# Kernel tuning notes

Hardware: AMD Instinct MI355X
Metric: run time of the kernel (lower is better)

## Reference

```python
import jax, jax.numpy as jnp
import numpy as np

EMBED_DIM = 512
NUM_HEADS = 8
HEAD_DIM = EMBED_DIM // NUM_HEADS
LN_EPS = 1e-5


def setup_inputs() -> dict:
    key = jax.random.key(0)
    ks = jax.random.split(key, 14)
    B, Lq, Lkv, E = 4, 1024, 4096, EMBED_DIM
    s = 0.02
    return {
        "query": jax.random.normal(ks[0], (B, Lq, E), dtype=jnp.float32),
        "key_value": jax.random.normal(ks[1], (B, Lkv, E), dtype=jnp.float32),
        "w_q": jax.random.normal(ks[2], (E, E), dtype=jnp.float32) * s,
        "w_k": jax.random.normal(ks[3], (E, E), dtype=jnp.float32) * s,
        "w_v": jax.random.normal(ks[4], (E, E), dtype=jnp.float32) * s,
        "b_q": jnp.zeros((E,), dtype=jnp.float32),
        "b_k": jnp.zeros((E,), dtype=jnp.float32),
        "b_v": jnp.zeros((E,), dtype=jnp.float32),
        "w_o": jax.random.normal(ks[5], (E, E), dtype=jnp.float32) * s,
        "b_o": jnp.zeros((E,), dtype=jnp.float32),
        "ln_gamma": jnp.ones((E,), dtype=jnp.float32),
        "ln_beta": jnp.zeros((E,), dtype=jnp.float32),
    }


def reference(query, key_value, w_q, w_k, w_v, b_q, b_k, b_v, w_o, b_o, ln_gamma, ln_beta):
    # query: [B, Lq, E]; key_value: [B, Lkv, E]
    B, Lq, E = query.shape
    Lkv = key_value.shape[1]
    H, D = NUM_HEADS, HEAD_DIM

    q = (query @ w_q.T + b_q).reshape(B, Lq, H, D)
    k = (key_value @ w_k.T + b_k).reshape(B, Lkv, H, D)
    v = (key_value @ w_v.T + b_v).reshape(B, Lkv, H, D)

    scale = 1.0 / jnp.sqrt(jnp.asarray(D, dtype=query.dtype))
    scores = jnp.einsum("bqhd,bkhd->bhqk", q, k) * scale  # [B,H,Lq,Lkv]
    attn = jax.nn.softmax(scores, axis=-1)
    # attn dropout off (eval mode)

    ctx = jnp.einsum("bhqk,bkhd->bqhd", attn, v).reshape(B, Lq, E)
    attn_output = ctx @ w_o.T + b_o
    # post-attn dropout off (eval mode)

    x = query + attn_output
    mu = jnp.mean(x, axis=-1, keepdims=True)
    var = jnp.mean(jnp.square(x - mu), axis=-1, keepdims=True)
    out = (x - mu) / jnp.sqrt(var + LN_EPS) * ln_gamma + ln_beta

    # need_weights=True: PyTorch averages attention weights over heads
    attn_weights = jnp.mean(attn, axis=1)  # [B, Lq, Lkv]
    return out, attn_weights
```

## Files before the change

kernel.cpp:

```cpp
#include <hip/hip_runtime.h>
#include <hip/hip_bf16.h>

namespace {

constexpr int E_DIM = 512;
constexpr int NH = 8;
constexpr int HD = 64;
constexpr int LQ = 1024;
constexpr int LKV = 4096;
constexpr int NB = 4;
constexpr int SPLIT = 4;
constexpr int SLICE = LKV / SPLIT;
constexpr int SSPLIT = 8;
constexpr size_t CPL = (size_t)NB * LQ * E_DIM;

typedef __attribute__((ext_vector_type(8))) short bf16x8;
typedef __attribute__((ext_vector_type(8))) unsigned short u16x8;
typedef __attribute__((ext_vector_type(4))) float f32x4;

typedef const unsigned int __attribute__((address_space(1)))* gptr1;
typedef unsigned int __attribute__((address_space(3)))* lptr3;

__device__ __forceinline__ void gl16(const unsigned short* g, unsigned short* l) {
  __builtin_amdgcn_global_load_lds((gptr1)g, (lptr3)l, 16, 0, 0);
}

__device__ __forceinline__ f32x4 mfma16(bf16x8 a, bf16x8 b, f32x4 c) {
  return __builtin_amdgcn_mfma_f32_16x16x32_bf16(a, b, c, 0, 0, 0);
}

__device__ __forceinline__ unsigned short f2b(float f) {
  unsigned int u = __float_as_uint(f);
  u += 0x7FFFu + ((u >> 16) & 1u);
  return (unsigned short)(u >> 16);
}

__device__ __forceinline__ float b2f(short s) {
  return __uint_as_float(((unsigned int)(unsigned short)s) << 16);
}

__device__ __forceinline__ unsigned int cvt_pk_bf16(float a, float b) {
  unsigned int r;
  asm("v_cvt_pk_bf16_f32 %0, %1, %2" : "=v"(r) : "v"(a), "v"(b));
  return r;
}

__global__ __launch_bounds__(256) void cvt_bf16(const float* __restrict__ s,
                                                unsigned short* __restrict__ d) {
  const int i = blockIdx.x * 256 + threadIdx.x;
  const float4 a = ((const float4*)s)[i * 2];
  const float4 b = ((const float4*)s)[i * 2 + 1];
  uint4 o;
  o.x = cvt_pk_bf16(a.x, a.y);
  o.y = cvt_pk_bf16(a.z, a.w);
  o.z = cvt_pk_bf16(b.x, b.y);
  o.w = cvt_pk_bf16(b.z, b.w);
  ((uint4*)d)[i] = o;
}

__global__ __launch_bounds__(256) void cvt_w4(const float* __restrict__ w0,
                                              const float* __restrict__ w1,
                                              const float* __restrict__ w2,
                                              const float* __restrict__ w3,
                                              unsigned short* __restrict__ d) {
  const float* s = blockIdx.y == 0 ? w0 : blockIdx.y == 1 ? w1
                   : blockIdx.y == 2 ? w2 : w3;
  unsigned short* dst = d + (size_t)blockIdx.y * (E_DIM * E_DIM);
  const int i = blockIdx.x * 256 + threadIdx.x;
  const float4 a = ((const float4*)s)[i * 2];
  const float4 b = ((const float4*)s)[i * 2 + 1];
  uint4 o;
  o.x = cvt_pk_bf16(a.x, a.y);
  o.y = cvt_pk_bf16(a.z, a.w);
  o.z = cvt_pk_bf16(b.x, b.y);
  o.w = cvt_pk_bf16(b.z, b.w);
  ((uint4*)dst)[i] = o;
}

template <int EPI>
__global__ __launch_bounds__(256) void gemm_bf16(
    const unsigned short* __restrict__ A, const unsigned short* __restrict__ B,
    const float* __restrict__ bias, void* __restrict__ outp, int L,
    float oscale) {
  __shared__ __align__(16) unsigned short As[128][32];
  __shared__ __align__(16) unsigned short Bs[128][32];
  const int tid = threadIdx.x;
  const int wv = tid >> 6, lane = tid & 63, lg = lane >> 4, lr = lane & 15;
  const int gx = gridDim.x, gy = gridDim.y;
  const int p = blockIdx.x + gx * blockIdx.y;
  const int xcd = p & 7, ii = p >> 3;
  const int by = xcd * (gy >> 3) + ii / gx;
  const int bx = ii - (ii / gx) * gx;
  const int i0 = by * 128, j0 = bx * 128;
  const int wm = wv >> 1, wn = wv & 1;
  const int srow = tid >> 2, scol = (tid & 3) * 8;
  f32x4 acc[4][4] = {};
  const unsigned short* ap = A + (size_t)(i0 + srow) * E_DIM + scol;
  const unsigned short* bp = B + (size_t)(j0 + srow) * E_DIM + scol;
  unsigned short* lA = &As[srow][scol];
  unsigned short* lB = &Bs[srow][scol];
  for (int k0 = 0; k0 < E_DIM; k0 += 32) {
    __syncthreads();
    gl16(ap + k0, lA);
    gl16(ap + k0 + (size_t)64 * E_DIM, lA + 64 * 32);
    gl16(bp + k0, lB);
    gl16(bp + k0 + (size_t)64 * E_DIM, lB + 64 * 32);
    __syncthreads();
    bf16x8 af[4], bg[4];
    for (int m = 0; m < 4; ++m)
      af[m] = *(const bf16x8*)&As[wm * 64 + m * 16 + lr][lg * 8];
    for (int n = 0; n < 4; ++n)
      bg[n] = *(const bf16x8*)&Bs[wn * 64 + n * 16 + lr][lg * 8];
    for (int m = 0; m < 4; ++m)
      for (int n = 0; n < 4; ++n)
        acc[m][n] = mfma16(af[m], bg[n], acc[m][n]);
  }
  for (int m = 0; m < 4; ++m)
    for (int n = 0; n < 4; ++n) {
      const int j = j0 + wn * 64 + n * 16 + lr;
      const float bj = bias[j];
      for (int r = 0; r < 4; ++r) {
        const int i = i0 + wm * 64 + m * 16 + lg * 4 + r;
        const float v = (acc[m][n][r] + bj) * oscale;
        if (EPI == 2) {
          ((float*)outp)[(size_t)i * E_DIM + j] = v;
        } else {
          const int bb = i / L, li = i - bb * L;
          const int hh = j >> 6, dd = j & 63;
          if (EPI == 0)
            ((unsigned short*)outp)[((size_t)(bb * NH + hh) * L + li) * HD + dd] = f2b(v);
          else
            ((unsigned short*)outp)[((size_t)(bb * NH + hh) * HD + dd) * L + li] = f2b(v);
        }
      }
    }
}

__global__ __launch_bounds__(512, 2) void attn_sums(
    const unsigned short* __restrict__ Qb, const unsigned short* __restrict__ Kb,
    float* __restrict__ l_part) {
  const int tid = threadIdx.x;
  const int h = tid >> 6, lane = tid & 63, lg = lane >> 4, lr = lane & 15;
  const int p = blockIdx.x + 16 * blockIdx.y + 64 * blockIdx.z;
  const int xcd = p & 7, ii = p >> 3;
  const int combo = xcd * 4 + (ii >> 4);
  const int q0 = (ii & 15) * 64;
  const int b = combo >> 3, sp = combo & 7;
  const size_t bh = (size_t)b * NH + h;
  const unsigned short* Qp = Qb + (bh * LQ + q0) * HD;
  const unsigned short* Kp = Kb + (bh * LKV + sp * (LKV / SSPLIT)) * HD;
  bf16x8 qB[4][2];
  for (int qs = 0; qs < 4; ++qs)
    for (int kk = 0; kk < 2; ++kk)
      qB[qs][kk] = *(const bf16x8*)(Qp + (qs * 16 + lr) * HD + kk * 32 + lg * 8);
  float qsum[4] = {};
  for (int t = 0; t < (LKV / SSPLIT) / 64; ++t) {
    const unsigned short* base = Kp + (size_t)t * 64 * HD;
    for (int k2h = 0; k2h < 2; ++k2h) {
      bf16x8 kA[2][2];
      for (int k2 = 0; k2 < 2; ++k2)
        for (int kk = 0; kk < 2; ++kk)
          kA[k2][kk] = *(const bf16x8*)(base + ((k2h * 2 + k2) * 16 + lr) * HD +
                                        kk * 32 + lg * 8);
      f32x4 sacc[2][4] = {};
      for (int k2 = 0; k2 < 2; ++k2)
        for (int qs = 0; qs < 4; ++qs)
          sacc[k2][qs] = mfma16(kA[k2][1], qB[qs][1],
                                mfma16(kA[k2][0], qB[qs][0], sacc[k2][qs]));
      for (int k2 = 0; k2 < 2; ++k2)
        for (int qs = 0; qs < 4; ++qs)
          for (int r = 0; r < 4; ++r)
            qsum[qs] += __builtin_amdgcn_exp2f(sacc[k2][qs][r]);
    }
  }
  for (int qs = 0; qs < 4; ++qs) {
    float v = qsum[qs];
    v += __shfl_xor(v, 16);
    v += __shfl_xor(v, 32);
    if (lg == 0)
      l_part[(size_t)sp * (NB * NH * LQ) + bh * LQ + q0 + qs * 16 + lr] = v;
  }
}

__global__ __launch_bounds__(512) void attn_main(
    const unsigned short* __restrict__ Qb, const unsigned short* __restrict__ Kb,
    const unsigned short* __restrict__ Vt, const float* __restrict__ l_part,
    float* __restrict__ attn_w, unsigned short* __restrict__ ctxp) {
  __shared__ __align__(16) unsigned short P[2][NH][64][72];
  const int tid = threadIdx.x;
  const int h = tid >> 6, lane = tid & 63, lg = lane >> 4, lr = lane & 15;
  const int p = blockIdx.x + 16 * blockIdx.y + 64 * blockIdx.z;
  const int xcd = p & 7, ii = p >> 3;
  const int combo = xcd * 2 + (ii >> 4);
  const int q0 = (ii & 15) * 64;
  const int b = combo >> 2, sp = combo & 3;
  const size_t bh = (size_t)b * NH + h;
  const unsigned short* Qp = Qb + (bh * LQ + q0) * HD;
  const unsigned short* Kp = Kb + bh * LKV * HD;
  const unsigned short* Vp = Vt + bh * HD * LKV;

  bf16x8 qB[4][2];
  for (int qs = 0; qs < 4; ++qs)
    for (int kk = 0; kk < 2; ++kk)
      qB[qs][kk] = *(const bf16x8*)(Qp + (qs * 16 + lr) * HD + kk * 32 + lg * 8);
  float nlg[4];
  for (int qs = 0; qs < 4; ++qs) {
    float ls = 0.f;
    for (int s = 0; s < SSPLIT; ++s)
      ls += l_part[(size_t)s * (NB * NH * LQ) + bh * LQ + q0 + qs * 16 + lr];
    nlg[qs] = -__builtin_amdgcn_logf(ls);
  }

  f32x4 cacc[4][4] = {};
  for (int t = 0; t < SLICE / 64; ++t) {
    const int kv0 = sp * SLICE + t * 64;
    unsigned short (*Pb)[64][72] = P[t & 1];
    bf16x8 vf[4][2];
    for (int ds = 0; ds < 4; ++ds)
      for (int kk = 0; kk < 2; ++kk)
        vf[ds][kk] = *(const bf16x8*)(Vp + (size_t)(ds * 16 + lr) * LKV + kv0 +
                                      kk * 32 + lg * 8);
    for (int kh = 0; kh < 2; ++kh) {
      bf16x8 kA[2][2];
      for (int k2 = 0; k2 < 2; ++k2)
        for (int kk = 0; kk < 2; ++kk)
          kA[k2][kk] = *(const bf16x8*)(Kp + (size_t)(kv0 + (kh * 2 + k2) * 16 + lr) * HD +
                                        kk * 32 + lg * 8);
      f32x4 sacc[2][4] = {};
      for (int k2 = 0; k2 < 2; ++k2)
        for (int qs = 0; qs < 4; ++qs)
          sacc[k2][qs] = mfma16(kA[k2][1], qB[qs][1],
                                mfma16(kA[k2][0], qB[qs][0], sacc[k2][qs]));
      for (int k2 = 0; k2 < 2; ++k2)
        for (int qs = 0; qs < 4; ++qs) {
          const int q = qs * 16 + lr;
          const float p0 = __builtin_amdgcn_exp2f(sacc[k2][qs][0] + nlg[qs]);
          const float p1 = __builtin_amdgcn_exp2f(sacc[k2][qs][1] + nlg[qs]);
          const float p2 = __builtin_amdgcn_exp2f(sacc[k2][qs][2] + nlg[qs]);
          const float p3 = __builtin_amdgcn_exp2f(sacc[k2][qs][3] + nlg[qs]);
          uint2 w;
          w.x = cvt_pk_bf16(p0, p1);
          w.y = cvt_pk_bf16(p2, p3);
          *(uint2*)&Pb[h][q][(kh * 2 + k2) * 16 + lg * 4] = w;
        }
    }
    for (int kk = 0; kk < 2; ++kk) {
      bf16x8 pa[4];
      for (int qs = 0; qs < 4; ++qs)
        pa[qs] = *(const bf16x8*)&Pb[h][qs * 16 + lr][kk * 32 + lg * 8];
      for (int qs = 0; qs < 4; ++qs)
        for (int ds = 0; ds < 4; ++ds)
          cacc[qs][ds] = mfma16(pa[qs], vf[ds][kk], cacc[qs][ds]);
    }
    __syncthreads();
    {
      const int qa = tid >> 3, La = tid & 7;
      float s[8] = {};
      for (int hh = 0; hh < NH; ++hh) {
        const bf16x8 v = *(const bf16x8*)&Pb[hh][qa][La * 8];
        for (int j = 0; j < 8; ++j) s[j] += b2f(v[j]);
      }
      float* op = attn_w + (size_t)(b * LQ + q0 + qa) * LKV + kv0 + La * 8;
      float4 o0 = {s[0] * 0.125f, s[1] * 0.125f, s[2] * 0.125f, s[3] * 0.125f};
      float4 o1 = {s[4] * 0.125f, s[5] * 0.125f, s[6] * 0.125f, s[7] * 0.125f};
      *(float4*)op = o0;
      *(float4*)(op + 4) = o1;
    }
  }
  unsigned short* cp = ctxp + (size_t)sp * CPL;
  for (int qs = 0; qs < 4; ++qs)
    for (int ds = 0; ds < 4; ++ds)
      for (int r = 0; r < 4; ++r)
        cp[(size_t)(b * LQ + q0 + qs * 16 + lg * 4 + r) * E_DIM + h * HD +
           ds * 16 + lr] = f2b(cacc[qs][ds][r]);
}

__global__ __launch_bounds__(256) void combine_ctx(
    const unsigned short* __restrict__ ctxp, unsigned short* __restrict__ ctxb) {
  const size_t i = (size_t)blockIdx.x * 256 + threadIdx.x;
  float s[8] = {};
  for (int pl = 0; pl < SPLIT; ++pl) {
    const bf16x8 v = ((const bf16x8*)(ctxp + pl * CPL))[i];
    for (int j = 0; j < 8; ++j) s[j] += b2f(v[j]);
  }
  uint4 o;
  o.x = cvt_pk_bf16(s[0], s[1]);
  o.y = cvt_pk_bf16(s[2], s[3]);
  o.z = cvt_pk_bf16(s[4], s[5]);
  o.w = cvt_pk_bf16(s[6], s[7]);
  ((uint4*)ctxb)[i] = o;
}

__global__ __launch_bounds__(256) void ln_kernel(
    const float* __restrict__ q, const float* __restrict__ ao,
    const float* __restrict__ gamma, const float* __restrict__ beta,
    float* __restrict__ out) {
  const int row = blockIdx.x;
  const int tid = threadIdx.x;
  const size_t base = (size_t)row * E_DIM;
  const float x0 = q[base + tid] + ao[base + tid];
  const float x1 = q[base + 256 + tid] + ao[base + 256 + tid];
  float s = x0 + x1, ss = x0 * x0 + x1 * x1;
  for (int off = 32; off >= 1; off >>= 1) {
    s += __shfl_down(s, off);
    ss += __shfl_down(ss, off);
  }
  __shared__ float ps[4], pss[4];
  if ((tid & 63) == 0) {
    ps[tid >> 6] = s;
    pss[tid >> 6] = ss;
  }
  __syncthreads();
  s = ps[0] + ps[1] + ps[2] + ps[3];
  ss = pss[0] + pss[1] + pss[2] + pss[3];
  const float mu = s * (1.f / E_DIM);
  float var = ss * (1.f / E_DIM) - mu * mu;
  var = fmaxf(var, 0.f);
  const float rstd = rsqrtf(var + 1e-5f);
  out[base + tid] = (x0 - mu) * rstd * gamma[tid] + beta[tid];
  out[base + 256 + tid] = (x1 - mu) * rstd * gamma[256 + tid] + beta[256 + tid];
}

}

extern "C" void kernel_launch(void* const* d_in, const int* in_sizes, int n_in,
                              void* d_out, int out_size, void* d_ws, size_t ws_size,
                              hipStream_t stream) {
  const float* query = (const float*)d_in[0];
  const float* key_value = (const float*)d_in[1];
  const float* w_q = (const float*)d_in[2];
  const float* w_k = (const float*)d_in[3];
  const float* w_v = (const float*)d_in[4];
  const float* b_q = (const float*)d_in[5];
  const float* b_k = (const float*)d_in[6];
  const float* b_v = (const float*)d_in[7];
  const float* w_o = (const float*)d_in[8];
  const float* b_o = (const float*)d_in[9];
  const float* ln_g = (const float*)d_in[10];
  const float* ln_b = (const float*)d_in[11];

  unsigned short* Qb = (unsigned short*)d_ws;
  unsigned short* Kb = Qb + 2097152;
  unsigned short* Vt = Kb + 8388608;
  float* l_part = (float*)(Vt + 8388608);
  unsigned short* Wb = (unsigned short*)(l_part + 262144);
  float* ao = (float*)(Wb + 1048576);
  unsigned short* KVb = (unsigned short*)(ao + 2097152);
  unsigned short* ctxp = KVb;
  unsigned short* Qxb = KVb + 8388608;
  unsigned short* ctxb = Qxb;

  float* out = (float*)d_out;
  float* attn_w = out + (size_t)NB * LQ * E_DIM;

  const float qscale = 0.125f * 1.44269504088896340736f;

  cvt_bf16<<<dim3(4096), dim3(256), 0, stream>>>(key_value, KVb);
  cvt_bf16<<<dim3(1024), dim3(256), 0, stream>>>(query, Qxb);
  cvt_w4<<<dim3(128, 4), dim3(256), 0, stream>>>(w_q, w_k, w_v, w_o, Wb);

  gemm_bf16<0><<<dim3(4, 32), dim3(256), 0, stream>>>(Qxb, Wb, b_q, Qb, LQ, qscale);
  gemm_bf16<0><<<dim3(4, 128), dim3(256), 0, stream>>>(KVb, Wb + 262144, b_k, Kb,
                                                       LKV, 1.0f);
  gemm_bf16<1><<<dim3(4, 128), dim3(256), 0, stream>>>(KVb, Wb + 524288, b_v, Vt,
                                                       LKV, 1.0f);

  attn_sums<<<dim3(16, NB, SSPLIT), dim3(512), 0, stream>>>(Qb, Kb, l_part);
  attn_main<<<dim3(16, NB, SPLIT), dim3(512), 0, stream>>>(Qb, Kb, Vt, l_part,
                                                           attn_w, ctxp);
  combine_ctx<<<dim3(1024), dim3(256), 0, stream>>>(ctxp, ctxb);
  gemm_bf16<2><<<dim3(4, 32), dim3(256), 0, stream>>>(ctxb, Wb + 786432, b_o, ao,
                                                      LQ, 1.0f);
  ln_kernel<<<dim3(NB * LQ), dim3(256), 0, stream>>>(query, ao, ln_g, ln_b, out);
}
```

Before: 257.0 us.

## Double KV split in attention, single-buffer P for occupancy, merge conversion kernels

Doubles the KV split of attn_main from 4 to 8 slices, which doubles the grid. The per-block LDS buffer for P is single-buffered, with an extra barrier, so that two 512-thread blocks can fit per CU, and the kernel requests that with launch bounds. The three fp32-to-bf16 conversion kernels are merged into one launch, and the bf16 unpacking in the head-average and combine steps uses plain bit masks. In exchange, combine_ctx reads twice as many partial contexts, the larger partial buffer spills over the staged query copy (so ctxb is moved onto Qb), and each tile adds a sync.

```diff
diff --git a/kernel.cpp b/kernel.cpp
--- a/kernel.cpp
+++ b/kernel.cpp
@@ -9,7 +9,7 @@
 constexpr int LQ = 1024;
 constexpr int LKV = 4096;
 constexpr int NB = 4;
-constexpr int SPLIT = 4;
+constexpr int SPLIT = 8;
 constexpr int SLICE = LKV / SPLIT;
 constexpr int SSPLIT = 8;
 constexpr size_t CPL = (size_t)NB * LQ * E_DIM;
@@ -35,46 +35,43 @@
   return (unsigned short)(u >> 16);
 }
 
-__device__ __forceinline__ float b2f(short s) {
-  return __uint_as_float(((unsigned int)(unsigned short)s) << 16);
-}
-
 __device__ __forceinline__ unsigned int cvt_pk_bf16(float a, float b) {
   unsigned int r;
   asm("v_cvt_pk_bf16_f32 %0, %1, %2" : "=v"(r) : "v"(a), "v"(b));
   return r;
 }
 
-__global__ __launch_bounds__(256) void cvt_bf16(const float* __restrict__ s,
-                                                unsigned short* __restrict__ d) {
-  const int i = blockIdx.x * 256 + threadIdx.x;
-  const float4 a = ((const float4*)s)[i * 2];
-  const float4 b = ((const float4*)s)[i * 2 + 1];
+__global__ __launch_bounds__(256) void cvt_all(
+    const float* __restrict__ query, const float* __restrict__ kv,
+    const float* __restrict__ w0, const float* __restrict__ w1,
+    const float* __restrict__ w2, const float* __restrict__ w3,
+    unsigned short* __restrict__ Qxb, unsigned short* __restrict__ KVb,
+    unsigned short* __restrict__ Wb) {
+  const int blk = blockIdx.x;
+  const float* s;
+  unsigned short* d;
+  size_t idx;
+  if (blk < 1024) {
+    idx = ((size_t)blk * 256 + threadIdx.x) * 8;
+    s = query; d = Qxb;
+  } else if (blk < 5120) {
+    idx = ((size_t)(blk - 1024) * 256 + threadIdx.x) * 8;
+    s = kv; d = KVb;
+  } else {
+    idx = ((size_t)(blk - 5120) * 256 + threadIdx.x) * 8;
+    const int widx = (int)(idx >> 18);
+    s = widx == 0 ? w0 : widx == 1 ? w1 : widx == 2 ? w2 : w3;
+    d = Wb;
+    s -= (size_t)widx << 18;
+  }
+  const float4 a = *(const float4*)(s + idx);
+  const float4 b = *(const float4*)(s + idx + 4);
   uint4 o;
   o.x = cvt_pk_bf16(a.x, a.y);
   o.y = cvt_pk_bf16(a.z, a.w);
   o.z = cvt_pk_bf16(b.x, b.y);
   o.w = cvt_pk_bf16(b.z, b.w);
-  ((uint4*)d)[i] = o;
-}
-
-__global__ __launch_bounds__(256) void cvt_w4(const float* __restrict__ w0,
-                                              const float* __restrict__ w1,
-                                              const float* __restrict__ w2,
-                                              const float* __restrict__ w3,
-                                              unsigned short* __restrict__ d) {
-  const float* s = blockIdx.y == 0 ? w0 : blockIdx.y == 1 ? w1
-                   : blockIdx.y == 2 ? w2 : w3;
-  unsigned short* dst = d + (size_t)blockIdx.y * (E_DIM * E_DIM);
-  const int i = blockIdx.x * 256 + threadIdx.x;
-  const float4 a = ((const float4*)s)[i * 2];
-  const float4 b = ((const float4*)s)[i * 2 + 1];
-  uint4 o;
-  o.x = cvt_pk_bf16(a.x, a.y);
-  o.y = cvt_pk_bf16(a.z, a.w);
-  o.z = cvt_pk_bf16(b.x, b.y);
-  o.w = cvt_pk_bf16(b.z, b.w);
-  ((uint4*)dst)[i] = o;
+  *(uint4*)(d + idx) = o;
 }
 
 template <int EPI>
@@ -182,18 +179,18 @@
   }
 }
 
-__global__ __launch_bounds__(512) void attn_main(
+__global__ __launch_bounds__(512, 2) void attn_main(
     const unsigned short* __restrict__ Qb, const unsigned short* __restrict__ Kb,
     const unsigned short* __restrict__ Vt, const float* __restrict__ l_part,
     float* __restrict__ attn_w, unsigned short* __restrict__ ctxp) {
-  __shared__ __align__(16) unsigned short P[2][NH][64][72];
+  __shared__ __align__(16) unsigned short P[NH][64][72];
   const int tid = threadIdx.x;
   const int h = tid >> 6, lane = tid & 63, lg = lane >> 4, lr = lane & 15;
   const int p = blockIdx.x + 16 * blockIdx.y + 64 * blockIdx.z;
   const int xcd = p & 7, ii = p >> 3;
-  const int combo = xcd * 2 + (ii >> 4);
+  const int combo = xcd * 4 + (ii >> 4);
   const int q0 = (ii & 15) * 64;
-  const int b = combo >> 2, sp = combo & 3;
+  const int b = combo >> 3, sp = combo & 7;
   const size_t bh = (size_t)b * NH + h;
   const unsigned short* Qp = Qb + (bh * LQ + q0) * HD;
   const unsigned short* Kp = Kb + bh * LKV * HD;
@@ -214,7 +211,6 @@
   f32x4 cacc[4][4] = {};
   for (int t = 0; t < SLICE / 64; ++t) {
     const int kv0 = sp * SLICE + t * 64;
-    unsigned short (*Pb)[64][72] = P[t & 1];
     bf16x8 vf[4][2];
     for (int ds = 0; ds < 4; ++ds)
       for (int kk = 0; kk < 2; ++kk)
@@ -241,31 +237,40 @@
           uint2 w;
           w.x = cvt_pk_bf16(p0, p1);
           w.y = cvt_pk_bf16(p2, p3);
-          *(uint2*)&Pb[h][q][(kh * 2 + k2) * 16 + lg * 4] = w;
+          *(uint2*)&P[h][q][(kh * 2 + k2) * 16 + lg * 4] = w;
         }
     }
+    __syncthreads();
     for (int kk = 0; kk < 2; ++kk) {
       bf16x8 pa[4];
       for (int qs = 0; qs < 4; ++qs)
-        pa[qs] = *(const bf16x8*)&Pb[h][qs * 16 + lr][kk * 32 + lg * 8];
+        pa[qs] = *(const bf16x8*)&P[h][qs * 16 + lr][kk * 32 + lg * 8];
       for (int qs = 0; qs < 4; ++qs)
         for (int ds = 0; ds < 4; ++ds)
           cacc[qs][ds] = mfma16(pa[qs], vf[ds][kk], cacc[qs][ds]);
     }
-    __syncthreads();
     {
       const int qa = tid >> 3, La = tid & 7;
-      float s[8] = {};
+      float2 s01 = {0.f, 0.f}, s23 = {0.f, 0.f}, s45 = {0.f, 0.f},
+             s67 = {0.f, 0.f};
       for (int hh = 0; hh < NH; ++hh) {
-        const bf16x8 v = *(const bf16x8*)&Pb[hh][qa][La * 8];
-        for (int j = 0; j < 8; ++j) s[j] += b2f(v[j]);
+        const uint4 v = *(const uint4*)&P[hh][qa][La * 8];
+        s01.x += __uint_as_float(v.x << 16);
+        s01.y += __uint_as_float(v.x & 0xFFFF0000u);
+        s23.x += __uint_as_float(v.y << 16);
+        s23.y += __uint_as_float(v.y & 0xFFFF0000u);
+        s45.x += __uint_as_float(v.z << 16);
+        s45.y += __uint_as_float(v.z & 0xFFFF0000u);
+        s67.x += __uint_as_float(v.w << 16);
+        s67.y += __uint_as_float(v.w & 0xFFFF0000u);
       }
       float* op = attn_w + (size_t)(b * LQ + q0 + qa) * LKV + kv0 + La * 8;
-      float4 o0 = {s[0] * 0.125f, s[1] * 0.125f, s[2] * 0.125f, s[3] * 0.125f};
-      float4 o1 = {s[4] * 0.125f, s[5] * 0.125f, s[6] * 0.125f, s[7] * 0.125f};
+      float4 o0 = {s01.x * 0.125f, s01.y * 0.125f, s23.x * 0.125f, s23.y * 0.125f};
+      float4 o1 = {s45.x * 0.125f, s45.y * 0.125f, s67.x * 0.125f, s67.y * 0.125f};
       *(float4*)op = o0;
       *(float4*)(op + 4) = o1;
     }
+    __syncthreads();
   }
   unsigned short* cp = ctxp + (size_t)sp * CPL;
   for (int qs = 0; qs < 4; ++qs)
@@ -278,16 +283,23 @@
 __global__ __launch_bounds__(256) void combine_ctx(
     const unsigned short* __restrict__ ctxp, unsigned short* __restrict__ ctxb) {
   const size_t i = (size_t)blockIdx.x * 256 + threadIdx.x;
-  float s[8] = {};
+  float2 s01 = {0.f, 0.f}, s23 = {0.f, 0.f}, s45 = {0.f, 0.f}, s67 = {0.f, 0.f};
   for (int pl = 0; pl < SPLIT; ++pl) {
-    const bf16x8 v = ((const bf16x8*)(ctxp + pl * CPL))[i];
-    for (int j = 0; j < 8; ++j) s[j] += b2f(v[j]);
+    const uint4 v = ((const uint4*)(ctxp + pl * CPL))[i];
+    s01.x += __uint_as_float(v.x << 16);
+    s01.y += __uint_as_float(v.x & 0xFFFF0000u);
+    s23.x += __uint_as_float(v.y << 16);
+    s23.y += __uint_as_float(v.y & 0xFFFF0000u);
+    s45.x += __uint_as_float(v.z << 16);
+    s45.y += __uint_as_float(v.z & 0xFFFF0000u);
+    s67.x += __uint_as_float(v.w << 16);
+    s67.y += __uint_as_float(v.w & 0xFFFF0000u);
   }
   uint4 o;
-  o.x = cvt_pk_bf16(s[0], s[1]);
-  o.y = cvt_pk_bf16(s[2], s[3]);
-  o.z = cvt_pk_bf16(s[4], s[5]);
-  o.w = cvt_pk_bf16(s[6], s[7]);
+  o.x = cvt_pk_bf16(s01.x, s01.y);
+  o.y = cvt_pk_bf16(s23.x, s23.y);
+  o.z = cvt_pk_bf16(s45.x, s45.y);
+  o.w = cvt_pk_bf16(s67.x, s67.y);
   ((uint4*)ctxb)[i] = o;
 }
 
@@ -340,24 +352,23 @@
   const float* ln_b = (const float*)d_in[11];
 
   unsigned short* Qb = (unsigned short*)d_ws;
-  unsigned short* Kb = Qb + 2097152;
-  unsigned short* Vt = Kb + 8388608;
-  float* l_part = (float*)(Vt + 8388608);
+  unsigned short* Kb = Qb + (size_t)2097152;
+  unsigned short* Vt = Kb + (size_t)8388608;
+  float* l_part = (float*)(Vt + (size_t)8388608);
   unsigned short* Wb = (unsigned short*)(l_part + 262144);
   float* ao = (float*)(Wb + 1048576);
   unsigned short* KVb = (unsigned short*)(ao + 2097152);
+  unsigned short* Qxb = KVb + (size_t)8388608;
   unsigned short* ctxp = KVb;
-  unsigned short* Qxb = KVb + 8388608;
-  unsigned short* ctxb = Qxb;
+  unsigned short* ctxb = Qb;
 
   float* out = (float*)d_out;
   float* attn_w = out + (size_t)NB * LQ * E_DIM;
 
   const float qscale = 0.125f * 1.44269504088896340736f;
 
-  cvt_bf16<<<dim3(4096), dim3(256), 0, stream>>>(key_value, KVb);
-  cvt_bf16<<<dim3(1024), dim3(256), 0, stream>>>(query, Qxb);
-  cvt_w4<<<dim3(128, 4), dim3(256), 0, stream>>>(w_q, w_k, w_v, w_o, Wb);
+  cvt_all<<<dim3(5632), dim3(256), 0, stream>>>(query, key_value, w_q, w_k, w_v,
+                                                w_o, Qxb, KVb, Wb);
 
   gemm_bf16<0><<<dim3(4, 32), dim3(256), 0, stream>>>(Qxb, Wb, b_q, Qb, LQ, qscale);
   gemm_bf16<0><<<dim3(4, 128), dim3(256), 0, stream>>>(KVb, Wb + 262144, b_k, Kb,
```

Result: slower. 265.5 us (+3.3%).
